# Performance work log

Hardware: AMD Instinct MI355X
Metric: run time of the kernel (lower is better)

The kernel has to match this reference:

```python
import jax, jax.numpy as jnp
import numpy as np

NR_EMB = 1024
B_COMMITMENT = 1.0


def setup_inputs() -> dict:
    key = jax.random.key(0)
    k1, k2 = jax.random.split(key)
    inpt = jax.random.normal(k1, (64, 2048, 64), dtype=jnp.float32)
    # VarianceScaling(uniform) over shape (D, K): limit = sqrt(3*scale/fan_in), scale=1, fan_in=D
    D = 64
    limit = np.sqrt(3.0 / D).astype(np.float32)
    emb_mtrx = jax.random.uniform(k2, (D, NR_EMB), dtype=jnp.float32, minval=-limit, maxval=limit)
    return {"inpt": inpt, "emb_mtrx": emb_mtrx}


def reference(inpt, emb_mtrx):
    D = inpt.shape[-1]
    x = inpt.reshape(-1, D)  # [N, D]
    dist = (jnp.sum(x * x, axis=1, keepdims=True)
            - 2.0 * (x @ emb_mtrx)
            + jnp.sum(emb_mtrx * emb_mtrx, axis=0, keepdims=True))
    idx = jnp.argmax(-dist, axis=1)  # [N]
    # avg_probs = mean of one-hot over N == normalized histogram (same math, no N x K one-hot)
    avg_probs = jnp.bincount(idx, length=NR_EMB).astype(inpt.dtype) / x.shape[0]
    perplexity = jnp.exp(-jnp.sum(avg_probs * jnp.log(avg_probs + 1e-10)))
    idx_nd = idx.reshape(inpt.shape[:-1])  # [B, T]
    q = jnp.take(emb_mtrx.T, idx_nd, axis=0)  # gather codebook rows -> [B, T, D]
    l_commitment = jnp.mean((jax.lax.stop_gradient(q) - inpt) ** 2)
    l_codebook = jnp.mean((q - jax.lax.stop_gradient(inpt)) ** 2)
    loss = B_COMMITMENT * l_commitment + l_codebook
    q = inpt + jax.lax.stop_gradient(q - inpt)  # straight-through estimator
    return q, loss, perplexity
```

## Files before the change

kernel.cpp:

```cpp
#include <hip/hip_runtime.h>

#define NROWS 131072
#define D 64
#define K 1024

typedef __attribute__((ext_vector_type(8))) short short8;
typedef __attribute__((ext_vector_type(4))) float f32x4;
typedef unsigned int u32;


__device__ __forceinline__ unsigned short f2bf_rne(float f) {
    u32 u = __float_as_uint(f);
    u += 0x7fff + ((u >> 16) & 1);
    return (unsigned short)(u >> 16);
}

__device__ __forceinline__ float b2f(short s) {
    return __uint_as_float(((u32)(unsigned short)s) << 16);
}

__global__ __launch_bounds__(256) void prep_kernel(const float* __restrict__ E,
                                                   unsigned short* __restrict__ ehT,
                                                   float* __restrict__ e2g,
                                                   int* __restrict__ hist) {
    __shared__ float ps[4][64];
    const int lane = threadIdx.x & 63;
    const int w = threadIdx.x >> 6;
    const int k = blockIdx.x * 64 + lane;
    float s = 0.f;
#pragma unroll
    for (int half = 0; half < 2; ++half) {
        short8 h8;
#pragma unroll
        for (int j = 0; j < 8; ++j) {
            float v = E[(w * 16 + half * 8 + j) * K + k];
            s = fmaf(v, v, s);
            h8[j] = (short)f2bf_rne(v);
        }
        *(short8*)(ehT + (size_t)k * D + w * 16 + half * 8) = h8;
    }
    ps[w][lane] = s;
    __syncthreads();
    if (w == 0) e2g[k] = -0.5f * (ps[0][lane] + ps[1][lane] + ps[2][lane] + ps[3][lane]);
    if (threadIdx.x < 64) hist[blockIdx.x * 64 + threadIdx.x] = 0;
}

__global__ __launch_bounds__(1024) void score_kernel(const float* __restrict__ X,
                                                     const unsigned short* __restrict__ ehT,
                                                     const float* __restrict__ e2g,
                                                     int* __restrict__ hist,
                                                     float* __restrict__ wavesum,
                                                     float* __restrict__ q) {
    __shared__ unsigned short xbuf[2][8192];
    __shared__ float mrg[2][128 * 17];
    __shared__ int idxl[256];
    __shared__ float redL[16];

    const int tid = threadIdx.x;
    const int wave = tid >> 6;
    const int lane = tid & 63;
    const int quad = lane >> 4;
    const int lc = lane & 15;
    const size_t row0 = (size_t)blockIdx.x * 256;

    const int st = tid >> 7, so = (tid >> 4) & 7, sl = tid & 15;
    const float* sbase = X + (row0 + (size_t)(st * 16 + sl)) * D + so * 8;
#pragma unroll
    for (int c = 0; c < 2; ++c) {
        float4 La = *(const float4*)(sbase + c * 8192);
        float4 Lb = *(const float4*)(sbase + c * 8192 + 4);
        union { u32 u[4]; short8 v; } pk;
        pk.u[0] = __builtin_amdgcn_perm(__float_as_uint(La.y), __float_as_uint(La.x), 0x07060302);
        pk.u[1] = __builtin_amdgcn_perm(__float_as_uint(La.w), __float_as_uint(La.z), 0x07060302);
        pk.u[2] = __builtin_amdgcn_perm(__float_as_uint(Lb.y), __float_as_uint(Lb.x), 0x07060302);
        pk.u[3] = __builtin_amdgcn_perm(__float_as_uint(Lb.w), __float_as_uint(Lb.z), 0x07060302);
        *(short8*)((char*)&xbuf[c][0] + tid * 16) = pk.v;
    }

    const int cbase = wave * 64;
    short8 ae[4][2];
    f32x4 e2f[4];
#pragma unroll
    for (int ct = 0; ct < 4; ++ct) {
        const unsigned short* ap = ehT + ((size_t)(cbase + ct * 16 + lc) << 6) + quad * 8;
        ae[ct][0] = *(const short8*)(ap);
        ae[ct][1] = *(const short8*)(ap + 32);
        e2f[ct] = *(const f32x4*)(e2g + cbase + ct * 16 + quad * 4);
    }
    const u32 cb0 = (u32)(cbase + quad * 4);

    __syncthreads();

    auto compute = [&](int c) {
        const char* bb = (const char*)&xbuf[c][0];
#pragma unroll 2
        for (int t = 0; t < 8; ++t) {
            const char* bp = bb + t * 2048 + quad * 256 + lc * 16;
            short8 b0 = *(const short8*)(bp);
            short8 b1 = *(const short8*)(bp + 1024);
            float bt = -3.4e38f;
#pragma unroll
            for (int ct = 0; ct < 4; ++ct) {
                f32x4 acc = __builtin_amdgcn_mfma_f32_16x16x32_bf16(ae[ct][0], b0, e2f[ct], 0, 0, 0);
                acc = __builtin_amdgcn_mfma_f32_16x16x32_bf16(ae[ct][1], b1, acc, 0, 0, 0);
                float p0 = __uint_as_float((__float_as_uint(acc[0]) & 0xFFFFFC00u) | (cb0 + ct * 16 + 0));
                float p1 = __uint_as_float((__float_as_uint(acc[1]) & 0xFFFFFC00u) | (cb0 + ct * 16 + 1));
                float p2 = __uint_as_float((__float_as_uint(acc[2]) & 0xFFFFFC00u) | (cb0 + ct * 16 + 2));
                float p3 = __uint_as_float((__float_as_uint(acc[3]) & 0xFFFFFC00u) | (cb0 + ct * 16 + 3));
                bt = fmaxf(bt, fmaxf(p0, p1));
                bt = fmaxf(bt, fmaxf(p2, p3));
            }
            bt = fmaxf(bt, __shfl_xor(bt, 16, 64));
            bt = fmaxf(bt, __shfl_xor(bt, 32, 64));
            if (lane < 16) mrg[c][(t * 16 + lane) * 17 + wave] = bt;
        }
    };

    auto merge = [&](int c) {
        if (tid < 128) {
            float m = mrg[c][tid * 17];
#pragma unroll
            for (int w = 1; w < 16; ++w) m = fmaxf(m, mrg[c][tid * 17 + w]);
            int kk = (int)(__float_as_uint(m) & 1023u);
            idxl[c * 128 + tid] = kk;
            atomicAdd(&hist[kk], 1);
        }
    };

    float ls = 0.f;
    const int er = tid >> 4, el = tid & 15;
    auto epilogue = [&](int h) {
#pragma unroll
        for (int it = 0; it < 2; ++it) {
            int rl = h * 128 + it * 64 + er;
            int k = idxl[rl];
            size_t row = row0 + rl;
            float4 xv = *(const float4*)(X + row * D + el * 4);
            short4 ev = *(const short4*)((const char*)ehT + (size_t)k * 128 + el * 8);
            float4 o;
            float dd;
            dd = b2f(ev.x) - xv.x; ls = fmaf(dd, dd, ls); o.x = xv.x + dd;
            dd = b2f(ev.y) - xv.y; ls = fmaf(dd, dd, ls); o.y = xv.y + dd;
            dd = b2f(ev.z) - xv.z; ls = fmaf(dd, dd, ls); o.z = xv.z + dd;
            dd = b2f(ev.w) - xv.w; ls = fmaf(dd, dd, ls); o.w = xv.w + dd;
            *(float4*)(q + row * D + el * 4) = o;
        }
    };

    compute(0);
    __syncthreads();
    merge(0);
    compute(1);
    __syncthreads();
    merge(1);
    epilogue(0);
    __syncthreads();
    epilogue(1);

    for (int off = 32; off > 0; off >>= 1) ls += __shfl_down(ls, off, 64);
    if (lane == 0) redL[wave] = ls;
    __syncthreads();
    if (tid == 0) {
        float L = 0.f;
#pragma unroll
        for (int i = 0; i < 16; ++i) L += redL[i];
        wavesum[blockIdx.x] = L;
    }
}

__global__ __launch_bounds__(1024) void finalize_kernel(const int* __restrict__ hist,
                                                        const float* __restrict__ wavesum,
                                                        float* __restrict__ out) {
    __shared__ float redH[16], redL[16];
    int tid = threadIdx.x;
    float p = (float)hist[tid] * (1.0f / (float)NROWS);
    float term = p * logf(p + 1e-10f);
    float ls = (tid < 512) ? wavesum[tid] : 0.f;
    for (int off = 32; off > 0; off >>= 1) {
        term += __shfl_down(term, off, 64);
        ls += __shfl_down(ls, off, 64);
    }
    int lane = tid & 63, wid = tid >> 6;
    if (lane == 0) { redH[wid] = term; redL[wid] = ls; }
    __syncthreads();
    if (tid == 0) {
        float H = 0.f, L = 0.f;
#pragma unroll
        for (int i = 0; i < 16; ++i) { H += redH[i]; L += redL[i]; }
        out[(size_t)NROWS * D + 0] = 2.0f * (L / (float)(NROWS * D));
        out[(size_t)NROWS * D + 1] = expf(-H);
    }
}

extern "C" void kernel_launch(void* const* d_in, const int* in_sizes, int n_in,
                              void* d_out, int out_size, void* d_ws, size_t ws_size,
                              hipStream_t stream) {
    const float* X = (const float*)d_in[0];
    const float* E = (const float*)d_in[1];
    float* out = (float*)d_out;

    char* w = (char*)d_ws;
    unsigned short* ehT = (unsigned short*)(w + 0);
    float* e2g          = (float*)(w + 131072);
    int* hist           = (int*)(w + 135168);
    float* wavesum      = (float*)(w + 139264);

    prep_kernel<<<16, 256, 0, stream>>>(E, ehT, e2g, hist);
    score_kernel<<<512, 1024, 0, stream>>>(X, ehT, e2g, hist, wavesum, out);
    finalize_kernel<<<1, 1024, 0, stream>>>(hist, wavesum, out);
}
```

Measured before the change: 126.5 us.

## Use small 256-thread blocks over 128 rows, looping waves across codebook quarters

Restructures the score kernel from 1024-thread blocks of 256 rows to 256-thread blocks of 128 rows. Each of the four waves now walks four codebook chunks, reloading bf16 codebook fragments per chunk and keeping running per-row maxima in registers. This cuts the cross-wave merge from 16 to 4 entries and lowers LDS and barrier cost per block, which should help occupancy and scheduling flexibility. In exchange, codebook fragments are re-read from global/L2 for each chunk, and the launch grows to 1024 blocks, so the finalize kernel now reads all 1024 partial sums.

```diff
diff --git a/kernel.cpp b/kernel.cpp
--- a/kernel.cpp
+++ b/kernel.cpp
@@ -45,60 +45,64 @@
     if (threadIdx.x < 64) hist[blockIdx.x * 64 + threadIdx.x] = 0;
 }
 
-__global__ __launch_bounds__(1024) void score_kernel(const float* __restrict__ X,
-                                                     const unsigned short* __restrict__ ehT,
-                                                     const float* __restrict__ e2g,
-                                                     int* __restrict__ hist,
-                                                     float* __restrict__ wavesum,
-                                                     float* __restrict__ q) {
-    __shared__ unsigned short xbuf[2][8192];
-    __shared__ float mrg[2][128 * 17];
-    __shared__ int idxl[256];
-    __shared__ float redL[16];
+__global__ __launch_bounds__(256) void score_kernel(const float* __restrict__ X,
+                                                    const unsigned short* __restrict__ ehT,
+                                                    const float* __restrict__ e2g,
+                                                    int* __restrict__ hist,
+                                                    float* __restrict__ wavesum,
+                                                    float* __restrict__ q) {
+    __shared__ unsigned short xbuf[8192];
+    __shared__ float mrg[128 * 5];
+    __shared__ int idxl[128];
+    __shared__ float redL[4];
 
     const int tid = threadIdx.x;
     const int wave = tid >> 6;
     const int lane = tid & 63;
     const int quad = lane >> 4;
     const int lc = lane & 15;
-    const size_t row0 = (size_t)blockIdx.x * 256;
-
-    const int st = tid >> 7, so = (tid >> 4) & 7, sl = tid & 15;
-    const float* sbase = X + (row0 + (size_t)(st * 16 + sl)) * D + so * 8;
-#pragma unroll
-    for (int c = 0; c < 2; ++c) {
-        float4 La = *(const float4*)(sbase + c * 8192);
-        float4 Lb = *(const float4*)(sbase + c * 8192 + 4);
-        union { u32 u[4]; short8 v; } pk;
-        pk.u[0] = __builtin_amdgcn_perm(__float_as_uint(La.y), __float_as_uint(La.x), 0x07060302);
-        pk.u[1] = __builtin_amdgcn_perm(__float_as_uint(La.w), __float_as_uint(La.z), 0x07060302);
-        pk.u[2] = __builtin_amdgcn_perm(__float_as_uint(Lb.y), __float_as_uint(Lb.x), 0x07060302);
-        pk.u[3] = __builtin_amdgcn_perm(__float_as_uint(Lb.w), __float_as_uint(Lb.z), 0x07060302);
-        *(short8*)((char*)&xbuf[c][0] + tid * 16) = pk.v;
-    }
-
-    const int cbase = wave * 64;
-    short8 ae[4][2];
-    f32x4 e2f[4];
-#pragma unroll
-    for (int ct = 0; ct < 4; ++ct) {
-        const unsigned short* ap = ehT + ((size_t)(cbase + ct * 16 + lc) << 6) + quad * 8;
-        ae[ct][0] = *(const short8*)(ap);
-        ae[ct][1] = *(const short8*)(ap + 32);
-        e2f[ct] = *(const f32x4*)(e2g + cbase + ct * 16 + quad * 4);
-    }
-    const u32 cb0 = (u32)(cbase + quad * 4);
-
-    __syncthreads();
-
-    auto compute = [&](int c) {
-        const char* bb = (const char*)&xbuf[c][0];
+    const size_t row0 = (size_t)blockIdx.x * 128;
+
+#pragma unroll
+    for (int j = 0; j < 4; ++j) {
+        int u = tid + j * 256;
+        int tt = u >> 7, oo = (u >> 4) & 7, ll = u & 15;
+        const float* xp = X + (row0 + (size_t)(tt * 16 + ll)) * D + oo * 8;
+        float4 La = *(const float4*)(xp);
+        float4 Lb = *(const float4*)(xp + 4);
+        union { u32 uu[4]; short8 v; } pk;
+        pk.uu[0] = __builtin_amdgcn_perm(__float_as_uint(La.y), __float_as_uint(La.x), 0x07060302);
+        pk.uu[1] = __builtin_amdgcn_perm(__float_as_uint(La.w), __float_as_uint(La.z), 0x07060302);
+        pk.uu[2] = __builtin_amdgcn_perm(__float_as_uint(Lb.y), __float_as_uint(Lb.x), 0x07060302);
+        pk.uu[3] = __builtin_amdgcn_perm(__float_as_uint(Lb.w), __float_as_uint(Lb.z), 0x07060302);
+        *(short8*)((char*)&xbuf[0] + u * 16) = pk.v;
+    }
+    __syncthreads();
+
+    float bt8[8];
+#pragma unroll
+    for (int t = 0; t < 8; ++t) bt8[t] = -3.4e38f;
+
+#pragma unroll 1
+    for (int h = 0; h < 4; ++h) {
+        const int cg = h * 256 + wave * 64;
+        short8 ae[4][2];
+        f32x4 e2f[4];
+#pragma unroll
+        for (int ct = 0; ct < 4; ++ct) {
+            const unsigned short* ap = ehT + ((size_t)(cg + ct * 16 + lc) << 6) + quad * 8;
+            ae[ct][0] = *(const short8*)(ap);
+            ae[ct][1] = *(const short8*)(ap + 32);
+            e2f[ct] = *(const f32x4*)(e2g + cg + ct * 16 + quad * 4);
+        }
+        const u32 cb0 = (u32)(cg + quad * 4);
+
 #pragma unroll 2
         for (int t = 0; t < 8; ++t) {
-            const char* bp = bb + t * 2048 + quad * 256 + lc * 16;
+            const char* bp = (const char*)&xbuf[0] + t * 2048 + quad * 256 + lc * 16;
             short8 b0 = *(const short8*)(bp);
             short8 b1 = *(const short8*)(bp + 1024);
-            float bt = -3.4e38f;
+            float bt = bt8[t];
 #pragma unroll
             for (int ct = 0; ct < 4; ++ct) {
                 f32x4 acc = __builtin_amdgcn_mfma_f32_16x16x32_bf16(ae[ct][0], b0, e2f[ct], 0, 0, 0);
@@ -110,62 +114,50 @@
                 bt = fmaxf(bt, fmaxf(p0, p1));
                 bt = fmaxf(bt, fmaxf(p2, p3));
             }
-            bt = fmaxf(bt, __shfl_xor(bt, 16, 64));
-            bt = fmaxf(bt, __shfl_xor(bt, 32, 64));
-            if (lane < 16) mrg[c][(t * 16 + lane) * 17 + wave] = bt;
+            bt8[t] = bt;
         }
-    };
-
-    auto merge = [&](int c) {
-        if (tid < 128) {
-            float m = mrg[c][tid * 17];
-#pragma unroll
-            for (int w = 1; w < 16; ++w) m = fmaxf(m, mrg[c][tid * 17 + w]);
-            int kk = (int)(__float_as_uint(m) & 1023u);
-            idxl[c * 128 + tid] = kk;
-            atomicAdd(&hist[kk], 1);
-        }
-    };
+    }
+
+#pragma unroll
+    for (int t = 0; t < 8; ++t) {
+        float bt = bt8[t];
+        bt = fmaxf(bt, __shfl_xor(bt, 16, 64));
+        bt = fmaxf(bt, __shfl_xor(bt, 32, 64));
+        if (lane < 16) mrg[(t * 16 + lane) * 5 + wave] = bt;
+    }
+    __syncthreads();
+
+    if (tid < 128) {
+        float m = fmaxf(fmaxf(mrg[tid * 5 + 0], mrg[tid * 5 + 1]),
+                        fmaxf(mrg[tid * 5 + 2], mrg[tid * 5 + 3]));
+        int kk = (int)(__float_as_uint(m) & 1023u);
+        idxl[tid] = kk;
+        atomicAdd(&hist[kk], 1);
+    }
+    __syncthreads();
 
     float ls = 0.f;
     const int er = tid >> 4, el = tid & 15;
-    auto epilogue = [&](int h) {
-#pragma unroll
-        for (int it = 0; it < 2; ++it) {
-            int rl = h * 128 + it * 64 + er;
-            int k = idxl[rl];
-            size_t row = row0 + rl;
-            float4 xv = *(const float4*)(X + row * D + el * 4);
-            short4 ev = *(const short4*)((const char*)ehT + (size_t)k * 128 + el * 8);
-            float4 o;
-            float dd;
-            dd = b2f(ev.x) - xv.x; ls = fmaf(dd, dd, ls); o.x = xv.x + dd;
-            dd = b2f(ev.y) - xv.y; ls = fmaf(dd, dd, ls); o.y = xv.y + dd;
-            dd = b2f(ev.z) - xv.z; ls = fmaf(dd, dd, ls); o.z = xv.z + dd;
-            dd = b2f(ev.w) - xv.w; ls = fmaf(dd, dd, ls); o.w = xv.w + dd;
-            *(float4*)(q + row * D + el * 4) = o;
-        }
-    };
-
-    compute(0);
-    __syncthreads();
-    merge(0);
-    compute(1);
-    __syncthreads();
-    merge(1);
-    epilogue(0);
-    __syncthreads();
-    epilogue(1);
-
+#pragma unroll 2
+    for (int it = 0; it < 8; ++it) {
+        int rl = it * 16 + er;
+        int k = idxl[rl];
+        size_t row = row0 + rl;
+        float4 xv = *(const float4*)(X + row * D + el * 4);
+        short4 ev = *(const short4*)((const char*)ehT + (size_t)k * 128 + el * 8);
+        float4 o;
+        float dd;
+        dd = b2f(ev.x) - xv.x; ls = fmaf(dd, dd, ls); o.x = xv.x + dd;
+        dd = b2f(ev.y) - xv.y; ls = fmaf(dd, dd, ls); o.y = xv.y + dd;
+        dd = b2f(ev.z) - xv.z; ls = fmaf(dd, dd, ls); o.z = xv.z + dd;
+        dd = b2f(ev.w) - xv.w; ls = fmaf(dd, dd, ls); o.w = xv.w + dd;
+        *(float4*)(q + row * D + el * 4) = o;
+    }
     for (int off = 32; off > 0; off >>= 1) ls += __shfl_down(ls, off, 64);
     if (lane == 0) redL[wave] = ls;
     __syncthreads();
-    if (tid == 0) {
-        float L = 0.f;
-#pragma unroll
-        for (int i = 0; i < 16; ++i) L += redL[i];
-        wavesum[blockIdx.x] = L;
-    }
+    if (tid == 0)
+        wavesum[blockIdx.x] = redL[0] + redL[1] + redL[2] + redL[3];
 }
 
 __global__ __launch_bounds__(1024) void finalize_kernel(const int* __restrict__ hist,
@@ -175,7 +167,7 @@
     int tid = threadIdx.x;
     float p = (float)hist[tid] * (1.0f / (float)NROWS);
     float term = p * logf(p + 1e-10f);
-    float ls = (tid < 512) ? wavesum[tid] : 0.f;
+    float ls = wavesum[tid];
     for (int off = 32; off > 0; off >>= 1) {
         term += __shfl_down(term, off, 64);
         ls += __shfl_down(ls, off, 64);
@@ -206,6 +198,6 @@
     float* wavesum      = (float*)(w + 139264);
 
     prep_kernel<<<16, 256, 0, stream>>>(E, ehT, e2g, hist);
-    score_kernel<<<512, 1024, 0, stream>>>(X, ehT, e2g, hist, wavesum, out);
+    score_kernel<<<NROWS / 128, 256, 0, stream>>>(X, ehT, e2g, hist, wavesum, out);
     finalize_kernel<<<1, 1024, 0, stream>>>(hist, wavesum, out);
 }
```

After: 126.5 us. About the same (-0.0%).
